# Optimization experiments

Measured on AMD Instinct MI355X. Metric: run time of the kernel, lower is better.

## Reference

```python
import jax, jax.numpy as jnp
import numpy as np

D_MODEL = 1024
N_HEADS = 16
HEAD_DIM = 64
D_FF = 4096


def rmsnorm(x, w):
    eps = jnp.finfo(x.dtype).eps
    var = jnp.mean(jnp.square(x), axis=-1, keepdims=True)
    return x * jax.lax.rsqrt(var + eps) * w


def setup_inputs() -> dict:
    key = jax.random.key(0)
    ks = jax.random.split(key, 8)
    d, h, hd, dff = D_MODEL, N_HEADS, HEAD_DIM, D_FF
    s = 0.02
    return {
        "x": jax.random.normal(ks[0], (2, 2048, d), dtype=jnp.float32),
        "norm_w": jnp.ones((d,), dtype=jnp.float32),
        "Wq": jax.random.normal(ks[1], (d, h * hd), dtype=jnp.float32) * s,
        "Wk": jax.random.normal(ks[2], (d, h * hd), dtype=jnp.float32) * s,
        "Wv": jax.random.normal(ks[3], (d, h * hd), dtype=jnp.float32) * s,
        "Wo": jax.random.normal(ks[4], (h * hd, d), dtype=jnp.float32) * s,
        "W1": jax.random.normal(ks[5], (d, dff), dtype=jnp.float32) * s,
        "W2": jax.random.normal(ks[6], (dff, d), dtype=jnp.float32) * s,
    }


def reference(x, norm_w, Wq, Wk, Wv, Wo, W1, W2):
    B, T, d = x.shape
    h, hd = N_HEADS, HEAD_DIM
    scale = 1.0 / np.sqrt(hd)

    xn = rmsnorm(x, norm_w)

    # attention branch
    q = (xn @ Wq).reshape(B, T, h, hd).transpose(0, 2, 1, 3)  # [B,h,T,hd]
    k = (xn @ Wk).reshape(B, T, h, hd).transpose(0, 2, 1, 3)
    v = (xn @ Wv).reshape(B, T, h, hd).transpose(0, 2, 1, 3)
    attn = jnp.einsum("bhqd,bhkd->bhqk", q, k) * scale
    causal = jnp.tril(jnp.ones((T, T), dtype=bool))
    attn = jnp.where(causal, attn, -jnp.inf)
    attn = jax.nn.softmax(attn, axis=-1)
    out = jnp.einsum("bhqk,bhkd->bhqd", attn, v)
    out = out.transpose(0, 2, 1, 3).reshape(B, T, h * hd)
    attn_out = out @ Wo

    # FFN branch
    ffn_out = jax.nn.silu(xn @ W1) @ W2

    return x + attn_out + ffn_out
```

## Files before the change

### kernel.cpp

```cpp
#include <hip/hip_runtime.h>

#define DM   1024
#define DFF  4096
#define NH   16
#define HD   64
#define TT   2048
#define BT   4096
#define KC   5120

typedef unsigned short u16;
typedef unsigned int   u32;
typedef __attribute__((ext_vector_type(8))) short s16x8;
typedef __attribute__((ext_vector_type(4))) float f32x4;

__device__ __forceinline__ u16 f2bf(float f) {
  u32 u = __builtin_bit_cast(u32, f);
  u += 0x7fffu + ((u >> 16) & 1u);
  return (u16)(u >> 16);
}

__device__ __forceinline__ void gl2lds16(const void* g, void* l) {
  __builtin_amdgcn_global_load_lds((__attribute__((address_space(1))) void*)(g),
                                   (__attribute__((address_space(3))) void*)(l),
                                   16, 0, 0);
}

#define S_BARRIER() do { __builtin_amdgcn_s_barrier(); __builtin_amdgcn_sched_barrier(0); } while (0)
#define VMWAIT(n)   asm volatile("s_waitcnt vmcnt(" #n ")" ::: "memory")

__global__ __launch_bounds__(256) void rmsnorm_k(const float* __restrict__ x,
                                                 const float* __restrict__ w,
                                                 u16* __restrict__ xn) {
  const int row = blockIdx.x;
  const int t = threadIdx.x;
  const float4 v = ((const float4*)(x + (size_t)row * DM))[t];
  float ss = v.x*v.x + v.y*v.y + v.z*v.z + v.w*v.w;
  #pragma unroll
  for (int off = 32; off; off >>= 1) ss += __shfl_xor(ss, off, 64);
  __shared__ float red[4];
  if ((t & 63) == 0) red[t >> 6] = ss;
  __syncthreads();
  const float tot = red[0] + red[1] + red[2] + red[3];
  const float r = __builtin_amdgcn_rsqf(tot * (1.0f / DM) + 1.1920929e-7f);
  const float4 wv = ((const float4*)w)[t];
  u16* o = xn + (size_t)row * DM + t * 4;
  o[0] = f2bf(v.x * r * wv.x);
  o[1] = f2bf(v.y * r * wv.y);
  o[2] = f2bf(v.z * r * wv.z);
  o[3] = f2bf(v.w * r * wv.w);
}

__global__ __launch_bounds__(256) void wtrans_k(const float* __restrict__ W,
                                                u16* __restrict__ Wt,
                                                int K, int N, int pitch, int koff) {
  __shared__ float tile[32][33];
  const int n0 = blockIdx.x * 32, k0 = blockIdx.y * 32;
  const int tx = threadIdx.x, ty = threadIdx.y;
  #pragma unroll
  for (int i = 0; i < 4; ++i)
    tile[ty + i*8][tx] = W[(size_t)(k0 + ty + i*8) * N + n0 + tx];
  __syncthreads();
  #pragma unroll
  for (int i = 0; i < 4; ++i)
    Wt[(size_t)(n0 + ty + i*8) * pitch + koff + k0 + tx] = f2bf(tile[tx][ty + i*8]);
}

__global__ __launch_bounds__(512, 2) void gemm_fused(const u16* __restrict__ A,
                                                     const u16* __restrict__ Bt,
                                                     u16* __restrict__ qkb,
                                                     u16* __restrict__ vtg,
                                                     u16* __restrict__ acat) {
  const int K = 1024;
  __shared__ u16 sA[4 * 256 * 32];
  __shared__ u16 sB[4 * 256 * 32];
  const int t = threadIdx.x;
  const int lane = t & 63, wave = t >> 6;
  const int quad = lane >> 4, l4 = lane & 15;
  const int wy = wave >> 2, wx = wave & 3;
  const size_t mBase = (size_t)blockIdx.y * 256;
  const size_t nBase = (size_t)blockIdx.x * 256;

  const int srow = lane >> 2;
  const int scol = ((lane & 3) ^ ((lane >> 3) & 3)) * 8;
  const u16* Ag0 = A  + (mBase + (size_t)(wave*2 + 0)*16 + srow) * K + scol;
  const u16* Ag1 = A  + (mBase + (size_t)(wave*2 + 1)*16 + srow) * K + scol;
  const u16* Bg0 = Bt + (nBase + (size_t)(wave*2 + 0)*16 + srow) * K + scol;
  const u16* Bg1 = Bt + (nBase + (size_t)(wave*2 + 1)*16 + srow) * K + scol;
  char* dA0 = (char*)sA + (wave*2 + 0) * 1024;
  char* dA1 = (char*)sA + (wave*2 + 1) * 1024;
  char* dB0 = (char*)sB + (wave*2 + 0) * 1024;
  char* dB1 = (char*)sB + (wave*2 + 1) * 1024;

  const int qsw = (quad ^ ((l4 >> 1) & 3)) * 8;

  f32x4 acc[8][4];
  #pragma unroll
  for (int i = 0; i < 8; ++i)
    #pragma unroll
    for (int j = 0; j < 4; ++j)
      acc[i][j] = (f32x4)0.0f;

  auto issue = [&](int slot, int k0) {
    gl2lds16(Ag0 + k0, dA0 + slot*16384);
    gl2lds16(Ag1 + k0, dA1 + slot*16384);
    gl2lds16(Bg0 + k0, dB0 + slot*16384);
    gl2lds16(Bg1 + k0, dB1 + slot*16384);
  };

  auto compute = [&](int slot) {
    const u16* pA = sA + slot * 8192;
    const u16* pB = sB + slot * 8192;
    s16x8 bfr[4];
    #pragma unroll
    for (int nj = 0; nj < 4; ++nj)
      bfr[nj] = *(const s16x8*)&pB[(wx*64 + nj*16 + l4) * 32 + qsw];
    __builtin_amdgcn_s_setprio(1);
    #pragma unroll
    for (int mi = 0; mi < 8; ++mi) {
      const s16x8 af = *(const s16x8*)&pA[(wy*128 + mi*16 + l4) * 32 + qsw];
      #pragma unroll
      for (int nj = 0; nj < 4; ++nj)
        acc[mi][nj] = __builtin_amdgcn_mfma_f32_16x16x32_bf16(af, bfr[nj], acc[mi][nj], 0, 0, 0);
    }
    __builtin_amdgcn_s_setprio(0);
  };

  const int NT = K / 32;
  issue(0, 0); issue(1, 32);
  VMWAIT(4);
  S_BARRIER();
  for (int kt = 0; kt < NT - 2; ++kt) {
    issue((kt + 2) & 3, (kt + 2) * 32);
    compute(kt & 3);
    VMWAIT(4);
    S_BARRIER();
  }
  compute((NT - 2) & 3);
  VMWAIT(0); S_BARRIER();
  compute((NT - 1) & 3);

  #pragma unroll
  for (int i = 0; i < 8; ++i) {
    const size_t row0 = mBase + wy*128 + i*16 + quad*4;
    #pragma unroll
    for (int j = 0; j < 4; ++j) {
      const int col = (int)nBase + wx*64 + j*16 + l4;
      if (nBase < 1024) {
        #pragma unroll
        for (int rg = 0; rg < 4; ++rg)
          qkb[(row0 + rg) * 2048 + col] = f2bf(acc[i][j][rg] * 0.18033688011f);
      } else if (nBase < 2048) {
        #pragma unroll
        for (int rg = 0; rg < 4; ++rg)
          qkb[(row0 + rg) * 2048 + col] = f2bf(acc[i][j][rg]);
      } else if (nBase < 3072) {
        const int cv = col - 2048, hh = cv >> 6, dd = cv & 63;
        const int bb = (int)(row0 >> 11), t0 = (int)(row0 & 2047);
        ushort4 pk;
        pk.x = f2bf(acc[i][j][0]); pk.y = f2bf(acc[i][j][1]);
        pk.z = f2bf(acc[i][j][2]); pk.w = f2bf(acc[i][j][3]);
        *(ushort4*)(vtg + ((size_t)((bb*16 + hh)*64 + dd)) * 2048 + t0) = pk;
      } else {
        #pragma unroll
        for (int rg = 0; rg < 4; ++rg) {
          float v = acc[i][j][rg];
          v = v / (1.0f + __expf(-v));
          acat[(row0 + rg) * (size_t)KC + 1024 + (col - 3072)] = f2bf(v);
        }
      }
    }
  }
}

__global__ __launch_bounds__(256, 2) void gemm_final(const u16* __restrict__ A,
                                                     const u16* __restrict__ Bt,
                                                     const float* __restrict__ x,
                                                     float* __restrict__ out) {
  __shared__ u16 sA[4 * 64 * 32];
  __shared__ u16 sB[4 * 128 * 32];
  const int t = threadIdx.x;
  const int lane = t & 63, wave = t >> 6;
  const int quad = lane >> 4, l4 = lane & 15;
  const int wy = wave >> 1, wx = wave & 1;
  const size_t mBase = (size_t)blockIdx.y * 64;
  const size_t nBase = (size_t)blockIdx.x * 128;
  const int r  = t >> 2;
  const int c8 = ((t & 3) ^ ((t >> 3) & 3)) * 8;
  const int qsw = (quad ^ ((l4 >> 1) & 3)) * 8;
  const u16* Ag  = A  + (mBase + r) * KC + c8;
  const u16* Bg0 = Bt + (nBase + r) * KC + c8;
  const u16* Bg1 = Bg0 + (size_t)64 * KC;
  char* sAb = (char*)sA + (wave << 10);
  char* sBb = (char*)sB + (wave << 10);

  f32x4 acc[2][4];
  #pragma unroll
  for (int i = 0; i < 2; ++i)
    #pragma unroll
    for (int j = 0; j < 4; ++j)
      acc[i][j] = (f32x4)0.0f;

  auto issue = [&](int bf, int k0) {
    gl2lds16(Ag  + k0, sAb + bf*4096);
    gl2lds16(Bg0 + k0, sBb + bf*8192);
    gl2lds16(Bg1 + k0, sBb + bf*8192 + 4096);
  };

  auto compute = [&](int bf) {
    const u16* pA = sA + bf * 2048;
    const u16* pB = sB + bf * 4096;
    s16x8 af[2], bfr[4];
    #pragma unroll
    for (int i = 0; i < 2; ++i)
      af[i] = *(const s16x8*)&pA[(wy*32 + i*16 + l4) * 32 + qsw];
    #pragma unroll
    for (int j = 0; j < 4; ++j)
      bfr[j] = *(const s16x8*)&pB[(wx*64 + j*16 + l4) * 32 + qsw];
    #pragma unroll
    for (int i = 0; i < 2; ++i)
      #pragma unroll
      for (int j = 0; j < 4; ++j)
        acc[i][j] = __builtin_amdgcn_mfma_f32_16x16x32_bf16(af[i], bfr[j], acc[i][j], 0, 0, 0);
  };

  const int NIT = KC / 32;
  issue(0, 0); issue(1, 32); issue(2, 64);
  for (int kt = 0; kt < NIT - 2; ++kt) {
    VMWAIT(6);
    S_BARRIER();
    if (kt + 3 < NIT) issue((kt + 3) & 3, (kt + 3) * 32);
    compute(kt & 3);
  }
  VMWAIT(3); S_BARRIER(); compute((NIT - 2) & 3);
  VMWAIT(0); S_BARRIER(); compute((NIT - 1) & 3);

  #pragma unroll
  for (int i = 0; i < 2; ++i) {
    const size_t row0 = mBase + wy*32 + i*16 + quad*4;
    #pragma unroll
    for (int j = 0; j < 4; ++j) {
      const int col = (int)nBase + wx*64 + j*16 + l4;
      #pragma unroll
      for (int rg = 0; rg < 4; ++rg) {
        const size_t idx = (row0 + rg) * (size_t)DM + col;
        out[idx] = x[idx] + acc[i][j][rg];
      }
    }
  }
}

__global__ __launch_bounds__(128) void attn_k(const u16* __restrict__ qk,
                                              const u16* __restrict__ vtg,
                                              u16* __restrict__ acat) {
  const int bh = blockIdx.x, b = bh >> 4, h = bh & 15;
  const int qt = 63 - blockIdx.y;
  const int qw = qt * 32;
  const int wave = threadIdx.x >> 6, lane = threadIdx.x & 63;
  const int quad = lane >> 4, l4 = lane & 15;
  const u16* Qp = qk + (size_t)b * TT * 2048 + h * HD;
  const u16* Kp = Qp + 1024;
  const u16* Vp = vtg + (size_t)bh * 64 * 2048;

  __shared__ u16 Pb[2][32][72];
  __shared__ float Ob[32][68];
  __shared__ float Lb[32];

  s16x8 qf[2][2];
  #pragma unroll
  for (int mi = 0; mi < 2; ++mi)
    #pragma unroll
    for (int kf = 0; kf < 2; ++kf)
      qf[mi][kf] = *(const s16x8*)(Qp + (size_t)(qw + mi*16 + l4) * 2048 + kf*32 + quad*8);

  const s16x8 ones = {0x3F80,0x3F80,0x3F80,0x3F80,0x3F80,0x3F80,0x3F80,0x3F80};

  f32x4 o[2][4];
  f32x4 lacc[2];
  #pragma unroll
  for (int mi = 0; mi < 2; ++mi) {
    lacc[mi] = (f32x4)0.0f;
    #pragma unroll
    for (int ni = 0; ni < 4; ++ni) o[mi][ni] = (f32x4)0.0f;
  }

  const int n   = (qt + 2) >> 1;
  const int n0  = (n + 1) >> 1;
  const int kt0 = wave ? n0 : 0;
  const int kt1 = wave ? n : n0;

  for (int kt = kt0; kt < kt1; ++kt) {
    const int k0 = kt * 64;

    f32x4 st[4][2];
    #pragma unroll
    for (int nj = 0; nj < 4; ++nj) {
      const u16* kr = Kp + (size_t)(k0 + nj*16 + l4) * 2048 + quad*8;
      const s16x8 kf0 = *(const s16x8*)kr;
      const s16x8 kf1 = *(const s16x8*)(kr + 32);
      #pragma unroll
      for (int mi = 0; mi < 2; ++mi) {
        f32x4 a = (f32x4)0.0f;
        a = __builtin_amdgcn_mfma_f32_16x16x32_bf16(kf0, qf[mi][0], a, 0, 0, 0);
        a = __builtin_amdgcn_mfma_f32_16x16x32_bf16(kf1, qf[mi][1], a, 0, 0, 0);
        st[nj][mi] = a;
      }
    }

    s16x8 vb[2][4];
    #pragma unroll
    for (int kf2 = 0; kf2 < 2; ++kf2)
      #pragma unroll
      for (int ni = 0; ni < 4; ++ni)
        vb[kf2][ni] = *(const s16x8*)(Vp + (size_t)(ni*16 + l4) * 2048 + k0 + kf2*32 + quad*8);

    if (k0 + 63 > qw) {
      #pragma unroll
      for (int nj = 0; nj < 4; ++nj)
        #pragma unroll
        for (int mi = 0; mi < 2; ++mi)
          #pragma unroll
          for (int rg = 0; rg < 4; ++rg) {
            const int key = k0 + nj*16 + quad*4 + rg;
            const int q   = qw + mi*16 + l4;
            if (key > q) st[nj][mi][rg] = -1e30f;
          }
    }

    #pragma unroll
    for (int nj = 0; nj < 4; ++nj)
      #pragma unroll
      for (int mi = 0; mi < 2; ++mi) {
        float p0 = __builtin_amdgcn_exp2f(st[nj][mi][0]);
        float p1 = __builtin_amdgcn_exp2f(st[nj][mi][1]);
        float p2 = __builtin_amdgcn_exp2f(st[nj][mi][2]);
        float p3 = __builtin_amdgcn_exp2f(st[nj][mi][3]);
        uint2 w;
        w.x = __builtin_amdgcn_perm(__builtin_bit_cast(u32, p1),
                                    __builtin_bit_cast(u32, p0), 0x07060302u);
        w.y = __builtin_amdgcn_perm(__builtin_bit_cast(u32, p3),
                                    __builtin_bit_cast(u32, p2), 0x07060302u);
        *(uint2*)&Pb[wave][mi*16 + l4][nj*16 + quad*4] = w;
      }

    #pragma unroll
    for (int kf2 = 0; kf2 < 2; ++kf2) {
      s16x8 pa[2];
      #pragma unroll
      for (int mi = 0; mi < 2; ++mi)
        pa[mi] = *(const s16x8*)&Pb[wave][mi*16 + l4][kf2*32 + quad*8];
      #pragma unroll
      for (int mi = 0; mi < 2; ++mi) {
        lacc[mi] = __builtin_amdgcn_mfma_f32_16x16x32_bf16(pa[mi], ones, lacc[mi], 0, 0, 0);
        #pragma unroll
        for (int ni = 0; ni < 4; ++ni)
          o[mi][ni] = __builtin_amdgcn_mfma_f32_16x16x32_bf16(pa[mi], vb[kf2][ni], o[mi][ni], 0, 0, 0);
      }
    }
  }

  if (wave == 1) {
    #pragma unroll
    for (int mi = 0; mi < 2; ++mi)
      #pragma unroll
      for (int rg = 0; rg < 4; ++rg) {
        const int row = mi*16 + quad*4 + rg;
        #pragma unroll
        for (int ni = 0; ni < 4; ++ni) Ob[row][ni*16 + l4] = o[mi][ni][rg];
        if (l4 == 0) Lb[row] = lacc[mi][rg];
      }
  }
  __syncthreads();
  if (wave == 0) {
    #pragma unroll
    for (int mi = 0; mi < 2; ++mi)
      #pragma unroll
      for (int rg = 0; rg < 4; ++rg) {
        const int row = mi*16 + quad*4 + rg;
        const float inv = 1.0f / (lacc[mi][rg] + Lb[row]);
        #pragma unroll
        for (int ni = 0; ni < 4; ++ni)
          Pb[0][row][ni*16 + l4] = f2bf((o[mi][ni][rg] + Ob[row][ni*16 + l4]) * inv);
      }
    #pragma unroll
    for (int it = 0; it < 4; ++it) {
      const int row = it*8 + (lane >> 3);
      const int c0  = (lane & 7) * 8;
      const s16x8 pk = *(const s16x8*)&Pb[0][row][c0];
      *(s16x8*)(acat + ((size_t)b * TT + qw + row) * KC + h*HD + c0) = pk;
    }
  }
}

extern "C" void kernel_launch(void* const* d_in, const int* in_sizes, int n_in,
                              void* d_out, int out_size, void* d_ws, size_t ws_size,
                              hipStream_t stream) {
  (void)in_sizes; (void)n_in; (void)out_size; (void)ws_size;
  const float* x  = (const float*)d_in[0];
  const float* nw = (const float*)d_in[1];
  const float* Wq = (const float*)d_in[2];
  const float* Wk = (const float*)d_in[3];
  const float* Wv = (const float*)d_in[4];
  const float* Wo = (const float*)d_in[5];
  const float* W1 = (const float*)d_in[6];
  const float* W2 = (const float*)d_in[7];

  char* ws = (char*)d_ws;
  u16*   xn      = (u16*)(ws);
  u16*   wqkv1_t = (u16*)(ws + ((size_t)8  << 20));
  u16*   bcat    = (u16*)(ws + ((size_t)22 << 20));
  u16*   qkb     = (u16*)(ws + ((size_t)32 << 20));
  u16*   vtg     = (u16*)(ws + ((size_t)48 << 20));
  u16*   acat    = (u16*)(ws + ((size_t)56 << 20));
  float* dout    = (float*)d_out;

  rmsnorm_k<<<BT, 256, 0, stream>>>(x, nw, xn);
  const dim3 tb(32, 8);
  wtrans_k<<<dim3(32, 32),  tb, 0, stream>>>(Wq, wqkv1_t,                      1024, 1024, 1024, 0);
  wtrans_k<<<dim3(32, 32),  tb, 0, stream>>>(Wk, wqkv1_t + (size_t)1024*1024,  1024, 1024, 1024, 0);
  wtrans_k<<<dim3(32, 32),  tb, 0, stream>>>(Wv, wqkv1_t + (size_t)2048*1024,  1024, 1024, 1024, 0);
  wtrans_k<<<dim3(128, 32), tb, 0, stream>>>(W1, wqkv1_t + (size_t)3072*1024,  1024, 4096, 1024, 0);
  wtrans_k<<<dim3(32, 32),  tb, 0, stream>>>(Wo, bcat,                         1024, 1024, 5120, 0);
  wtrans_k<<<dim3(32, 128), tb, 0, stream>>>(W2, bcat,                         4096, 1024, 5120, 1024);

  gemm_fused<<<dim3(28, 16), 512, 0, stream>>>(xn, wqkv1_t, qkb, vtg, acat);
  attn_k<<<dim3(32, 64), 128, 0, stream>>>(qkb, vtg, acat);
  gemm_final<<<dim3(8, 64), 256, 0, stream>>>(acat, bcat, x, dout);
}
```

Measured before the change: 373.1 us.

## Restructure QKV GEMM mainloop into 8-phase ping-pong schedule with BK=64

Replaces the 4-slot BK=32 LDS ring in the fused QKV/FFN-up GEMM with a 2-slot BK=64 double buffer. Each k-tile is split into four quadrant phases that interleave LDS fragment reads, global-to-LDS prefetch of the next tile, and MFMA bursts, separated by barriers. The swizzle moves to an 8-chunk XOR pattern to match 64-wide rows. The aim is better overlap of memory and matrix work, with fewer LDS reads per MFMA. The cost is many more barriers per k-tile and a finely tuned wait-count scheme that could stall if mis-sequenced.

```diff
diff --git a/kernel.cpp b/kernel.cpp
--- a/kernel.cpp
+++ b/kernel.cpp
@@ -71,8 +71,8 @@
                                                      u16* __restrict__ vtg,
                                                      u16* __restrict__ acat) {
   const int K = 1024;
-  __shared__ u16 sA[4 * 256 * 32];
-  __shared__ u16 sB[4 * 256 * 32];
+  __shared__ u16 sA[2 * 16384];
+  __shared__ u16 sB[2 * 16384];
   const int t = threadIdx.x;
   const int lane = t & 63, wave = t >> 6;
   const int quad = lane >> 4, l4 = lane & 15;
@@ -80,18 +80,16 @@
   const size_t mBase = (size_t)blockIdx.y * 256;
   const size_t nBase = (size_t)blockIdx.x * 256;
 
-  const int srow = lane >> 2;
-  const int scol = ((lane & 3) ^ ((lane >> 3) & 3)) * 8;
-  const u16* Ag0 = A  + (mBase + (size_t)(wave*2 + 0)*16 + srow) * K + scol;
-  const u16* Ag1 = A  + (mBase + (size_t)(wave*2 + 1)*16 + srow) * K + scol;
-  const u16* Bg0 = Bt + (nBase + (size_t)(wave*2 + 0)*16 + srow) * K + scol;
-  const u16* Bg1 = Bt + (nBase + (size_t)(wave*2 + 1)*16 + srow) * K + scol;
-  char* dA0 = (char*)sA + (wave*2 + 0) * 1024;
-  char* dA1 = (char*)sA + (wave*2 + 1) * 1024;
-  char* dB0 = (char*)sB + (wave*2 + 0) * 1024;
-  char* dB1 = (char*)sB + (wave*2 + 1) * 1024;
-
-  const int qsw = (quad ^ ((l4 >> 1) & 3)) * 8;
+  const int grow = t >> 3;
+  const int gchk = ((t & 7) ^ (grow & 7)) * 8;
+  const u16* AgR = A  + (mBase + grow) * K + gchk;
+  const u16* BgR = Bt + (nBase + grow) * K + gchk;
+  char* dA = (char*)sA;
+  char* dB = (char*)sB;
+  const int woff = wave * 1024;
+
+  const int cs0 = ((quad)     ^ (l4 & 7)) * 8;
+  const int cs1 = ((4 + quad) ^ (l4 & 7)) * 8;
 
   f32x4 acc[8][4];
   #pragma unroll
@@ -100,44 +98,87 @@
     for (int j = 0; j < 4; ++j)
       acc[i][j] = (f32x4)0.0f;
 
-  auto issue = [&](int slot, int k0) {
-    gl2lds16(Ag0 + k0, dA0 + slot*16384);
-    gl2lds16(Ag1 + k0, dA1 + slot*16384);
-    gl2lds16(Bg0 + k0, dB0 + slot*16384);
-    gl2lds16(Bg1 + k0, dB1 + slot*16384);
-  };
-
-  auto compute = [&](int slot) {
-    const u16* pA = sA + slot * 8192;
-    const u16* pB = sB + slot * 8192;
-    s16x8 bfr[4];
-    #pragma unroll
-    for (int nj = 0; nj < 4; ++nj)
-      bfr[nj] = *(const s16x8*)&pB[(wx*64 + nj*16 + l4) * 32 + qsw];
-    __builtin_amdgcn_s_setprio(1);
-    #pragma unroll
-    for (int mi = 0; mi < 8; ++mi) {
-      const s16x8 af = *(const s16x8*)&pA[(wy*128 + mi*16 + l4) * 32 + qsw];
-      #pragma unroll
-      for (int nj = 0; nj < 4; ++nj)
-        acc[mi][nj] = __builtin_amdgcn_mfma_f32_16x16x32_bf16(af, bfr[nj], acc[mi][nj], 0, 0, 0);
-    }
-    __builtin_amdgcn_s_setprio(0);
-  };
-
-  const int NT = K / 32;
-  issue(0, 0); issue(1, 32);
-  VMWAIT(4);
+  s16x8 a[4][2], b[4][2];
+
+  #define STG(p, slot, kt) do {                                                  \
+    const int k0_ = (kt) * 64;                                                   \
+    if ((p) == 0) {                                                              \
+      gl2lds16(BgR + (size_t)0*64*K + k0_, dB + (slot)*32768 +     0 + woff);    \
+      gl2lds16(BgR + (size_t)1*64*K + k0_, dB + (slot)*32768 +  8192 + woff);    \
+    } else if ((p) == 1) {                                                       \
+      gl2lds16(BgR + (size_t)2*64*K + k0_, dB + (slot)*32768 + 16384 + woff);    \
+      gl2lds16(BgR + (size_t)3*64*K + k0_, dB + (slot)*32768 + 24576 + woff);    \
+    } else if ((p) == 2) {                                                       \
+      gl2lds16(AgR + (size_t)0*64*K + k0_, dA + (slot)*32768 +     0 + woff);    \
+      gl2lds16(AgR + (size_t)2*64*K + k0_, dA + (slot)*32768 + 16384 + woff);    \
+    } else {                                                                     \
+      gl2lds16(AgR + (size_t)1*64*K + k0_, dA + (slot)*32768 +  8192 + woff);    \
+      gl2lds16(AgR + (size_t)3*64*K + k0_, dA + (slot)*32768 + 24576 + woff);    \
+    }                                                                            \
+  } while (0)
+
+  #define RDA(slot, qm) do {                                                     \
+    const u16* p_ = sA + (slot)*16384 + wy*8192;                                 \
+    _Pragma("unroll")                                                            \
+    for (int m_ = 0; m_ < 4; ++m_) {                                             \
+      const int ro_ = (((qm)*4 + m_)*16 + l4) * 64;                              \
+      a[m_][0] = *(const s16x8*)&p_[ro_ + cs0];                                  \
+      a[m_][1] = *(const s16x8*)&p_[ro_ + cs1];                                  \
+    }                                                                            \
+  } while (0)
+
+  #define RDB(slot, qn) do {                                                     \
+    const u16* p_ = sB + (slot)*16384 + (wx>>1)*8192 + (wx&1)*4096;              \
+    _Pragma("unroll")                                                            \
+    for (int n_ = 0; n_ < 2; ++n_) {                                             \
+      const int ro_ = (((qn)*2 + n_)*16 + l4) * 64;                              \
+      b[(qn)*2 + n_][0] = *(const s16x8*)&p_[ro_ + cs0];                         \
+      b[(qn)*2 + n_][1] = *(const s16x8*)&p_[ro_ + cs1];                         \
+    }                                                                            \
+  } while (0)
+
+  #define MM(qm, qn) do {                                                        \
+    __builtin_amdgcn_s_setprio(1);                                               \
+    _Pragma("unroll")                                                            \
+    for (int m_ = 0; m_ < 4; ++m_)                                               \
+      _Pragma("unroll")                                                          \
+      for (int n_ = 0; n_ < 2; ++n_) {                                           \
+        acc[(qm)*4+m_][(qn)*2+n_] = __builtin_amdgcn_mfma_f32_16x16x32_bf16(     \
+            a[m_][0], b[(qn)*2+n_][0], acc[(qm)*4+m_][(qn)*2+n_], 0, 0, 0);      \
+        acc[(qm)*4+m_][(qn)*2+n_] = __builtin_amdgcn_mfma_f32_16x16x32_bf16(     \
+            a[m_][1], b[(qn)*2+n_][1], acc[(qm)*4+m_][(qn)*2+n_], 0, 0, 0);      \
+      }                                                                          \
+    __builtin_amdgcn_s_setprio(0);                                               \
+  } while (0)
+
+  STG(0, 0, 0); STG(1, 0, 0); STG(2, 0, 0); STG(3, 0, 0);
+  VMWAIT(2);
   S_BARRIER();
-  for (int kt = 0; kt < NT - 2; ++kt) {
-    issue((kt + 2) & 3, (kt + 2) * 32);
-    compute(kt & 3);
-    VMWAIT(4);
-    S_BARRIER();
-  }
-  compute((NT - 2) & 3);
-  VMWAIT(0); S_BARRIER();
-  compute((NT - 1) & 3);
+
+  for (int i = 0; i < 7; ++i) {
+    const int kt1 = 2*i + 1, kt2 = 2*i + 2;
+    RDA(0,0); RDB(0,0); STG(0,1,kt1); S_BARRIER(); MM(0,0);            S_BARRIER();
+    RDB(0,1);           STG(1,1,kt1); S_BARRIER(); MM(0,1); VMWAIT(4); S_BARRIER();
+    RDA(0,1);           STG(2,1,kt1); S_BARRIER(); MM(1,0);            S_BARRIER();
+                        STG(3,1,kt1); S_BARRIER(); MM(1,1); VMWAIT(2); S_BARRIER();
+    RDA(1,0); RDB(1,0); STG(0,0,kt2); S_BARRIER(); MM(0,0);            S_BARRIER();
+    RDB(1,1);           STG(1,0,kt2); S_BARRIER(); MM(0,1); VMWAIT(4); S_BARRIER();
+    RDA(1,1);           STG(2,0,kt2); S_BARRIER(); MM(1,0);            S_BARRIER();
+                        STG(3,0,kt2); S_BARRIER(); MM(1,1); VMWAIT(2); S_BARRIER();
+  }
+  RDA(0,0); RDB(0,0); STG(0,1,15); S_BARRIER(); MM(0,0);            S_BARRIER();
+  RDB(0,1);           STG(1,1,15); S_BARRIER(); MM(0,1); VMWAIT(4); S_BARRIER();
+  RDA(0,1);           STG(2,1,15); S_BARRIER(); MM(1,0);            S_BARRIER();
+                      STG(3,1,15); S_BARRIER(); MM(1,1); VMWAIT(2); S_BARRIER();
+  RDA(1,0); RDB(1,0);              S_BARRIER(); MM(0,0);            S_BARRIER();
+  RDB(1,1);                        S_BARRIER(); MM(0,1); VMWAIT(0); S_BARRIER();
+  RDA(1,1);                        S_BARRIER(); MM(1,0);            S_BARRIER();
+                                   S_BARRIER(); MM(1,1);            S_BARRIER();
+
+  #undef STG
+  #undef RDA
+  #undef RDB
+  #undef MM
 
   #pragma unroll
   for (int i = 0; i < 8; ++i) {
```

Result: faster. 361.6 us (-3.1%).
